# Kernel tuning notes

Hardware: AMD Instinct MI355X
Metric: run time of the kernel (lower is better)

The kernel has to match this reference:

```python
import jax, jax.numpy as jnp
import numpy as np

IN_FEATURES = 4096
OUT_FEATURES = 4096
SHARED_ROWS = 512
BATCH = 4096


def setup_inputs() -> dict:
    key = jax.random.key(0)
    k1, k2, k3 = jax.random.split(key, 3)
    x = jax.random.normal(k1, (BATCH, IN_FEATURES), dtype=jnp.float32)
    shared_weights = jax.random.normal(k2, (SHARED_ROWS, IN_FEATURES), dtype=jnp.float32)
    bias = jax.random.normal(k3, (OUT_FEATURES,), dtype=jnp.float32)
    return {"x": x, "shared_weights": shared_weights, "bias": bias}


def reference(x, shared_weights, bias):
    # Original: W = shared_weights.repeat(out_features // shared_rows, 1)  -> [out, in]
    #           y = x @ W.T + bias
    # Row i of W equals shared_weights[i % shared_rows], so the output columns are a
    # tile of the small GEMM result — compute the small GEMM once and tile (same math,
    # avoids materializing the full [out, in] weight).
    reps = OUT_FEATURES // SHARED_ROWS
    y_small = jnp.einsum("bi,ri->br", x, shared_weights)  # [batch, shared_rows]
    y = jnp.tile(y_small, (1, reps)) + bias  # [batch, out_features]
    return y
```

## Files before the change

kernel.cpp:

```cpp
#include <hip/hip_runtime.h>
#include <hip/hip_bf16.h>


typedef __bf16 bf8 __attribute__((ext_vector_type(8)));
typedef float f4 __attribute__((ext_vector_type(4)));
typedef unsigned int uint;
typedef unsigned short ushort;

constexpr int M = 4096;
constexpr int K = 4096;
constexpr int NS = 512;
constexpr int OUTF = 4096;
constexpr int BM = 64, BN = 64, BK = 64;
constexpr int NITER = K / BK;

#define PERM_HI2(hi, lo) __builtin_amdgcn_perm((hi), (lo), 0x07060302u)

__device__ __forceinline__ void async16(const ushort* g, ushort* l) {
  __builtin_amdgcn_global_load_lds(
      (const __attribute__((address_space(1))) void*)g,
      (__attribute__((address_space(3))) void*)l, 16, 0, 0);
}

__global__ __launch_bounds__(256)
void convert_kernel(const float* __restrict__ x, const float* __restrict__ w,
                    ushort* __restrict__ xb, ushort* __restrict__ wb) {
  const size_t i = (size_t)blockIdx.x * 256 + threadIdx.x;
  constexpr size_t NX = (size_t)M * K / 8;
  const float* src;
  ushort* dst;
  if (i < NX) { src = x + i * 8; dst = xb + i * 8; }
  else        { const size_t j = i - NX; src = w + j * 8; dst = wb + j * 8; }
  const uint4 a = *reinterpret_cast<const uint4*>(src);
  const uint4 b = *reinterpret_cast<const uint4*>(src + 4);
  uint4 o;
  o.x = PERM_HI2(a.y, a.x); o.y = PERM_HI2(a.w, a.z);
  o.z = PERM_HI2(b.y, b.x); o.w = PERM_HI2(b.w, b.z);
  *reinterpret_cast<uint4*>(dst) = o;
}

__global__ __launch_bounds__(256, 5)
void gemm_kernel(const ushort* __restrict__ xb, const ushort* __restrict__ wb,
                 const float* __restrict__ bias, float* __restrict__ out) {
  __shared__ __align__(16) ushort As[2][BM * BK];
  __shared__ __align__(16) ushort Bs[2][BN * BK];

  const int gid = blockIdx.x;
  const int nt = gid & 7;
  const int mt = gid >> 3;

  const int tid  = threadIdx.x;
  const int wv   = tid >> 6;
  const int lane = tid & 63;

  int goff[2], lloc[2];
#pragma unroll
  for (int j = 0; j < 2; ++j) {
    const int c = (wv * 2 + j) * 64 + lane;
    const int r = c >> 3;
    const int g = (c & 7) ^ (r & 7);
    goff[j] = r * K + g * 8;
    lloc[j] = (wv * 2 + j) * 512;
  }

  const ushort* xT = xb + (size_t)(mt * BM) * K;
  const ushort* wT = wb + (size_t)(nt * BN) * K;

  const int wm = (wv & 1) * 32;
  const int wn = (wv >> 1) * 32;
  const int lr = lane & 15;
  const int lq = lane >> 4;

  f4 acc[2][2] = {};

#pragma unroll
  for (int j = 0; j < 2; ++j) {
    async16(xT + goff[j], &As[0][lloc[j]]);
    async16(wT + goff[j], &Bs[0][lloc[j]]);
  }
  __syncthreads();

  for (int kk = 0; kk < NITER; ++kk) {
    const int cur = kk & 1;

    if (kk + 1 < NITER) {
      const int ko = (kk + 1) * BK;
#pragma unroll
      for (int j = 0; j < 2; ++j) {
        async16(xT + ko + goff[j], &As[cur ^ 1][lloc[j]]);
        async16(wT + ko + goff[j], &Bs[cur ^ 1][lloc[j]]);
      }
    }

#pragma unroll
    for (int t = 0; t < 2; ++t) {
      const int sc = ((t * 4 + lq) ^ (lr & 7)) * 8;
      bf8 af[2], bfv[2];
#pragma unroll
      for (int mf = 0; mf < 2; ++mf)
        af[mf] = *reinterpret_cast<const bf8*>(&As[cur][(wm + mf * 16 + lr) * BK + sc]);
#pragma unroll
      for (int nf = 0; nf < 2; ++nf)
        bfv[nf] = *reinterpret_cast<const bf8*>(&Bs[cur][(wn + nf * 16 + lr) * BK + sc]);
#pragma unroll
      for (int mf = 0; mf < 2; ++mf)
#pragma unroll
        for (int nf = 0; nf < 2; ++nf)
          acc[mf][nf] = __builtin_amdgcn_mfma_f32_16x16x32_bf16(af[mf], bfv[nf], acc[mf][nf], 0, 0, 0);
    }

    __syncthreads();
  }

  float bv[8][2];
#pragma unroll
  for (int rep = 0; rep < 8; ++rep)
#pragma unroll
    for (int nf = 0; nf < 2; ++nf)
      bv[rep][nf] = bias[rep * NS + nt * BN + wn + nf * 16 + lr];

  float* ob = out + (size_t)(mt * BM) * OUTF;
#pragma unroll
  for (int mf = 0; mf < 2; ++mf)
#pragma unroll
    for (int r = 0; r < 4; ++r) {
      const int row = wm + mf * 16 + lq * 4 + r;
#pragma unroll
      for (int nf = 0; nf < 2; ++nf) {
        const float v = acc[mf][nf][r];
        const int col0 = nt * BN + wn + nf * 16 + lr;
#pragma unroll
        for (int rep = 0; rep < 8; ++rep)
          ob[(size_t)row * OUTF + rep * NS + col0] = v + bv[rep][nf];
      }
    }
}

extern "C" void kernel_launch(void* const* d_in, const int* in_sizes, int n_in,
                              void* d_out, int out_size, void* d_ws, size_t ws_size,
                              hipStream_t stream) {
  (void)in_sizes; (void)n_in; (void)out_size; (void)ws_size;
  const float* x    = (const float*)d_in[0];
  const float* w    = (const float*)d_in[1];
  const float* bias = (const float*)d_in[2];
  float* out = (float*)d_out;

  ushort* xb = (ushort*)d_ws;
  ushort* wb = (ushort*)d_ws + (size_t)M * K;

  constexpr int conv_blocks = (int)(((size_t)M * K / 8 + (size_t)NS * K / 8) / 256);
  convert_kernel<<<dim3(conv_blocks), dim3(256), 0, stream>>>(x, w, xb, wb);
  gemm_kernel<<<dim3(64 * 8), dim3(256), 0, stream>>>(xb, wb, bias, out);
}
```

Baseline: 170.8 us.

## Triple-buffer GEMM K-loop, remap block order, stage epilogue through LDS

```diff
diff --git a/kernel.cpp b/kernel.cpp
--- a/kernel.cpp
+++ b/kernel.cpp
@@ -13,8 +13,11 @@
 constexpr int OUTF = 4096;
 constexpr int BM = 64, BN = 64, BK = 64;
 constexpr int NITER = K / BK;
+constexpr int SSTR = 68;
 
 #define PERM_HI2(hi, lo) __builtin_amdgcn_perm((hi), (lo), 0x07060302u)
+#define WAITCNT_VM4 0xF74
+#define WAITCNT_VM0 0xF70
 
 __device__ __forceinline__ void async16(const ushort* g, ushort* l) {
   __builtin_amdgcn_global_load_lds(
@@ -39,15 +42,15 @@
   *reinterpret_cast<uint4*>(dst) = o;
 }
 
-__global__ __launch_bounds__(256, 5)
+__global__ __launch_bounds__(256, 2)
 void gemm_kernel(const ushort* __restrict__ xb, const ushort* __restrict__ wb,
                  const float* __restrict__ bias, float* __restrict__ out) {
-  __shared__ __align__(16) ushort As[2][BM * BK];
-  __shared__ __align__(16) ushort Bs[2][BN * BK];
+  __shared__ __align__(16) ushort As[3][BM * BK];
+  __shared__ __align__(16) ushort Bs[3][BN * BK];
 
-  const int gid = blockIdx.x;
-  const int nt = gid & 7;
-  const int mt = gid >> 3;
+  const int b  = blockIdx.x;
+  const int mt = ((b >> 6) << 3) | (b & 7);
+  const int nt = (b >> 3) & 7;
 
   const int tid  = threadIdx.x;
   const int wv   = tid >> 6;
@@ -73,67 +76,85 @@
 
   f4 acc[2][2] = {};
 
+  auto issue = [&](int tile, int stage) {
+    const int ko = tile * BK;
 #pragma unroll
-  for (int j = 0; j < 2; ++j) {
-    async16(xT + goff[j], &As[0][lloc[j]]);
-    async16(wT + goff[j], &Bs[0][lloc[j]]);
-  }
-  __syncthreads();
+    for (int j = 0; j < 2; ++j) {
+      async16(xT + ko + goff[j], &As[stage][lloc[j]]);
+      async16(wT + ko + goff[j], &Bs[stage][lloc[j]]);
+    }
+  };
 
+  issue(0, 0);
+  issue(1, 1);
+
+  int st = 0;
   for (int kk = 0; kk < NITER; ++kk) {
-    const int cur = kk & 1;
+    if (kk + 1 < NITER) __builtin_amdgcn_s_waitcnt(WAITCNT_VM4);
+    else                __builtin_amdgcn_s_waitcnt(WAITCNT_VM0);
+    __builtin_amdgcn_s_barrier();
+    asm volatile("" ::: "memory");
 
-    if (kk + 1 < NITER) {
-      const int ko = (kk + 1) * BK;
-#pragma unroll
-      for (int j = 0; j < 2; ++j) {
-        async16(xT + ko + goff[j], &As[cur ^ 1][lloc[j]]);
-        async16(wT + ko + goff[j], &Bs[cur ^ 1][lloc[j]]);
-      }
+    if (kk + 2 < NITER) {
+      int st2 = st + 2; if (st2 >= 3) st2 -= 3;
+      issue(kk + 2, st2);
     }
 
+    const ushort* aT = As[st];
+    const ushort* bT = Bs[st];
 #pragma unroll
     for (int t = 0; t < 2; ++t) {
       const int sc = ((t * 4 + lq) ^ (lr & 7)) * 8;
       bf8 af[2], bfv[2];
 #pragma unroll
       for (int mf = 0; mf < 2; ++mf)
-        af[mf] = *reinterpret_cast<const bf8*>(&As[cur][(wm + mf * 16 + lr) * BK + sc]);
+        af[mf] = *reinterpret_cast<const bf8*>(&aT[(wm + mf * 16 + lr) * BK + sc]);
 #pragma unroll
       for (int nf = 0; nf < 2; ++nf)
-        bfv[nf] = *reinterpret_cast<const bf8*>(&Bs[cur][(wn + nf * 16 + lr) * BK + sc]);
+        bfv[nf] = *reinterpret_cast<const bf8*>(&bT[(wn + nf * 16 + lr) * BK + sc]);
 #pragma unroll
       for (int mf = 0; mf < 2; ++mf)
 #pragma unroll
         for (int nf = 0; nf < 2; ++nf)
           acc[mf][nf] = __builtin_amdgcn_mfma_f32_16x16x32_bf16(af[mf], bfv[nf], acc[mf][nf], 0, 0, 0);
     }
+    asm volatile("" ::: "memory");
 
-    __syncthreads();
+    if (++st >= 3) st = 0;
   }
 
-  float bv[8][2];
-#pragma unroll
-  for (int rep = 0; rep < 8; ++rep)
-#pragma unroll
-    for (int nf = 0; nf < 2; ++nf)
-      bv[rep][nf] = bias[rep * NS + nt * BN + wn + nf * 16 + lr];
-
-  float* ob = out + (size_t)(mt * BM) * OUTF;
+  __syncthreads();
+  float* sc = reinterpret_cast<float*>(&As[0][0]);
 #pragma unroll
   for (int mf = 0; mf < 2; ++mf)
 #pragma unroll
-    for (int r = 0; r < 4; ++r) {
-      const int row = wm + mf * 16 + lq * 4 + r;
+    for (int nf = 0; nf < 2; ++nf)
 #pragma unroll
-      for (int nf = 0; nf < 2; ++nf) {
-        const float v = acc[mf][nf][r];
-        const int col0 = nt * BN + wn + nf * 16 + lr;
+      for (int r = 0; r < 4; ++r)
+        sc[(wm + mf * 16 + lq * 4 + r) * SSTR + wn + nf * 16 + lr] = acc[mf][nf][r];
+  __syncthreads();
+
+  const int c4 = tid & 15;
+  const int r0 = (tid >> 4) * 4;
+  const float4* bias4 = reinterpret_cast<const float4*>(bias);
+  float4 bb[8];
 #pragma unroll
-        for (int rep = 0; rep < 8; ++rep)
-          ob[(size_t)row * OUTF + rep * NS + col0] = v + bv[rep][nf];
-      }
+  for (int rep = 0; rep < 8; ++rep)
+    bb[rep] = bias4[rep * 128 + nt * 16 + c4];
+
+#pragma unroll
+  for (int rr = 0; rr < 4; ++rr) {
+    const int row = r0 + rr;
+    const float4 v = *reinterpret_cast<const float4*>(&sc[row * SSTR + c4 * 4]);
+    float* orow = out + (size_t)(mt * BM + row) * OUTF + nt * BN + c4 * 4;
+#pragma unroll
+    for (int rep = 0; rep < 8; ++rep) {
+      float4 o;
+      o.x = v.x + bb[rep].x; o.y = v.y + bb[rep].y;
+      o.z = v.z + bb[rep].z; o.w = v.w + bb[rep].w;
+      *reinterpret_cast<float4*>(orow + rep * NS) = o;
     }
+  }
 }
 
 extern "C" void kernel_launch(void* const* d_in, const int* in_sizes, int n_in,
```

After: 162.6 us. 1.05x faster.
